# Kernel tuning notes

Hardware: AMD Instinct MI355X
Metric: run time of the kernel (lower is better)

## Reference

```python
import jax, jax.numpy as jnp
import numpy as np

N_QUBITS = 4
N_LAYERS = 2
ENT = [(i, (i + 1) % N_QUBITS) for i in range(N_QUBITS)]  # fixed entangling ring


def _ry(t):
    c, s = jnp.cos(t / 2), jnp.sin(t / 2)
    return jnp.stack([jnp.stack([c, -s]), jnp.stack([s, c])]).astype(jnp.complex64)


def _rx(t):
    c, s = jnp.cos(t / 2), jnp.sin(t / 2)
    return jnp.stack([jnp.stack([c + 0j, -1j * s]), jnp.stack([-1j * s, c + 0j])]).astype(jnp.complex64)


def _rz(t):
    e = jnp.exp(-0.5j * t.astype(jnp.complex64))
    z = jnp.zeros_like(e)
    return jnp.stack([jnp.stack([e, z]), jnp.stack([z, jnp.conj(e)])])


def _apply_1q(state, U, w):
    # state: (2,)*N_QUBITS; apply 2x2 U on wire w
    s = jnp.moveaxis(state, w, 0)
    s = jnp.tensordot(U, s, ((1,), (0,)))
    return jnp.moveaxis(s, 0, w)


def _cnot(state, c, t):
    s = jnp.moveaxis(state, (c, t), (0, 1))
    s = jnp.concatenate([s[:1], jnp.flip(s[1:], axis=1)], axis=0)
    return jnp.moveaxis(s, (0, 1), (c, t))


def _ansatz(state, vec, params):
    for i in range(N_QUBITS):
        state = _apply_1q(state, _ry(vec[i]), i)
    for l in range(N_LAYERS):
        for i in range(N_QUBITS):
            state = _apply_1q(state, _rx(params[l, i, 0]), i)
            state = _apply_1q(state, _ry(params[l, i, 1]), i)
            state = _apply_1q(state, _rz(params[l, i, 2]), i)
        for a_, b_ in ENT:
            state = _cnot(state, a_, b_)
    return state


def _adjoint_ansatz(state, vec, params):
    # inverse gates in reverse order
    for l in reversed(range(N_LAYERS)):
        for a_, b_ in reversed(ENT):
            state = _cnot(state, a_, b_)  # CNOT is self-inverse
        for i in reversed(range(N_QUBITS)):
            state = _apply_1q(state, _rz(-params[l, i, 2]), i)
            state = _apply_1q(state, _ry(-params[l, i, 1]), i)
            state = _apply_1q(state, _rx(-params[l, i, 0]), i)
    for i in reversed(range(N_QUBITS)):
        state = _apply_1q(state, _ry(-vec[i]), i)
    return state


def setup_inputs() -> dict:
    key = jax.random.key(0)
    k1, k2, k3 = jax.random.split(key, 3)
    a = jax.random.normal(k1, (1024, N_QUBITS), dtype=jnp.float32)
    b = jax.random.normal(k2, (1024, N_QUBITS), dtype=jnp.float32)
    params = jax.random.normal(k3, (N_LAYERS, N_QUBITS, 3), dtype=jnp.float32)
    return {"a": a, "b": b, "params": params}


def reference(a, b, params):
    def pair(x, y):
        psi = jnp.zeros((2,) * N_QUBITS, jnp.complex64).at[(0,) * N_QUBITS].set(1.0)
        psi = _ansatz(psi, x, params)
        psi = _adjoint_ansatz(psi, y, params)
        probs = jnp.abs(psi) ** 2
        # expval of PauliZ on wire 0: +1 for |0>, -1 for |1> on axis 0
        z = jnp.sum(probs[0]) - jnp.sum(probs[1])
        return jnp.abs(z)

    # Gram matrix [len(a), len(b)]
    return jax.vmap(lambda x: jax.vmap(lambda y: pair(x, y))(b))(a)
```

## Files before the change

### kernel.cpp

```cpp
#include <hip/hip_runtime.h>


#define NA 1024
#define NB 1024
#define RT2 1.41421356237f

typedef __attribute__((ext_vector_type(8))) short bf16x8;
typedef __attribute__((ext_vector_type(4))) float f32x4;

__device__ __forceinline__ unsigned short f2bf(float x) {
    union { float f; unsigned u; } v; v.f = x;
    unsigned r = v.u + 0x7fffu + ((v.u >> 16) & 1u);
    return (unsigned short)(r >> 16);
}

__device__ __forceinline__ uint4 pack8(const float* f) {
    uint4 u;
    u.x = (unsigned)f2bf(f[0]) | ((unsigned)f2bf(f[1]) << 16);
    u.y = (unsigned)f2bf(f[2]) | ((unsigned)f2bf(f[3]) << 16);
    u.z = (unsigned)f2bf(f[4]) | ((unsigned)f2bf(f[5]) << 16);
    u.w = (unsigned)f2bf(f[6]) | ((unsigned)f2bf(f[7]) << 16);
    return u;
}

__device__ __forceinline__ void ry_gate(float* sr, float* si, int w, float t) {
    float s, c; __sincosf(0.5f * t, &s, &c);
    int st = 8 >> w;
    #pragma unroll
    for (int b = 0; b < 16; ++b) {
        if (b & st) continue;
        int j = b | st;
        float r0 = sr[b], i0 = si[b], r1 = sr[j], i1 = si[j];
        sr[b] = c * r0 - s * r1;  si[b] = c * i0 - s * i1;
        sr[j] = s * r0 + c * r1;  si[j] = s * i0 + c * i1;
    }
}

__device__ __forceinline__ void rx_gate(float* sr, float* si, int w, float t) {
    float s, c; __sincosf(0.5f * t, &s, &c);
    int st = 8 >> w;
    #pragma unroll
    for (int b = 0; b < 16; ++b) {
        if (b & st) continue;
        int j = b | st;
        float r0 = sr[b], i0 = si[b], r1 = sr[j], i1 = si[j];
        sr[b] = c * r0 + s * i1;  si[b] = c * i0 - s * r1;
        sr[j] = c * r1 + s * i0;  si[j] = c * i1 - s * r0;
    }
}

__device__ __forceinline__ void rz_gate(float* sr, float* si, int w, float t) {
    float s, c; __sincosf(0.5f * t, &s, &c);
    int st = 8 >> w;
    #pragma unroll
    for (int b = 0; b < 16; ++b) {
        if (b & st) continue;
        int j = b | st;
        float r0 = sr[b], i0 = si[b], r1 = sr[j], i1 = si[j];
        sr[b] = c * r0 + s * i0;  si[b] = c * i0 - s * r0;
        sr[j] = c * r1 - s * i1;  si[j] = c * i1 + s * r1;
    }
}

__device__ __forceinline__ void cnot_gate(float* sr, float* si, int cw, int tw) {
    int cs = 8 >> cw, ts = 8 >> tw;
    #pragma unroll
    for (int b = 0; b < 16; ++b) {
        if ((b & cs) && !(b & ts)) {
            int j = b | ts;
            float tr = sr[b]; sr[b] = sr[j]; sr[j] = tr;
            float ti = si[b]; si[b] = si[j]; si[j] = ti;
        }
    }
}

__device__ __forceinline__ void ansatz(float* sr, float* si, const float* vec, const float* P) {
    #pragma unroll
    for (int q = 0; q < 4; ++q) ry_gate(sr, si, q, vec[q]);
    #pragma unroll
    for (int l = 0; l < 2; ++l) {
        #pragma unroll
        for (int q = 0; q < 4; ++q) {
            rx_gate(sr, si, q, P[l * 12 + q * 3 + 0]);
            ry_gate(sr, si, q, P[l * 12 + q * 3 + 1]);
            rz_gate(sr, si, q, P[l * 12 + q * 3 + 2]);
        }
        cnot_gate(sr, si, 0, 1);
        cnot_gate(sr, si, 1, 2);
        cnot_gate(sr, si, 2, 3);
        cnot_gate(sr, si, 3, 0);
    }
}

__global__ __launch_bounds__(512, 2) void qkm_fused(
    const float* __restrict__ a, const float* __restrict__ b,
    const float* __restrict__ params, float* __restrict__ out) {

    __shared__ float Wtr[64 * 136];
    __shared__ float Wti[64 * 136];
    __shared__ float Phr[64 * 17];
    __shared__ float Phi_[64 * 17];
    __shared__ __align__(16) char Qsb[32768];
    __shared__ __align__(16) char Msb[32768];

    const int tid = threadIdx.x;
    const int blk = blockIdx.x;
    const int xcd = blk & 7, slot = blk >> 3;
    const int bi = xcd * 2 + (slot >> 4);
    const int bj = slot & 15;
    const int row0 = bi * 64, col0 = bj * 64;

    float P[24];
    #pragma unroll
    for (int j = 0; j < 24; ++j) P[j] = params[j];

    const int y  = tid >> 3;
    const int k2 = tid & 7;
    const int k0 = k2 * 2;
    const int sy = (y & 15) << 4;

    {
        float sr[16], si[16];
        #pragma unroll
        for (int k = 0; k < 16; ++k) { sr[k] = (k == 8 + k2) ? 1.f : 0.f; si[k] = 0.f; }
        float vec[4];
        #pragma unroll
        for (int q = 0; q < 4; ++q) vec[q] = b[(col0 + y) * 4 + q];
        ansatz(sr, si, vec, P);
        float* wr = Wtr + y * 136 + k2 * 17;
        float* wi = Wti + y * 136 + k2 * 17;
        #pragma unroll
        for (int l = 0; l < 16; ++l) { wr[l] = sr[l]; wi[l] = si[l]; }
    }
    __syncthreads();

    if (tid < 64) {
        float sr[16], si[16];
        #pragma unroll
        for (int k = 0; k < 16; ++k) { sr[k] = (k == 0) ? 1.f : 0.f; si[k] = 0.f; }
        float vec[4];
        #pragma unroll
        for (int q = 0; q < 4; ++q) vec[q] = a[(row0 + tid) * 4 + q];
        ansatz(sr, si, vec, P);
        float* qr = Phr + tid * 17;
        float* qi = Phi_ + tid * 17;
        #pragma unroll
        for (int l = 0; l < 16; ++l) { qr[l] = sr[l]; qi[l] = si[l]; }
    }

    {
        const float* wyr = Wtr + y * 136;
        const float* wyi = Wti + y * 136;
        #pragma unroll
        for (int rr = 0; rr < 2; ++rr) {
            const int k = k0 + rr;
            float re[16], im[16];
            #pragma unroll
            for (int l = 0; l < 16; ++l) { re[l] = 0.f; im[l] = 0.f; }
            #pragma unroll
            for (int p2 = 0; p2 < 8; ++p2) {
                const float* br  = wyr + p2 * 17;
                const float* bi_ = wyi + p2 * 17;
                float ar = br[k], ai = bi_[k];
                #pragma unroll
                for (int l = 0; l < 16; ++l) {
                    float xr = br[l], xi = bi_[l];
                    re[l] += ar * xr + ai * xi;
                    im[l] += xi * ar - xr * ai;
                }
            }
            float row[16];
            #pragma unroll
            for (int l = 0; l < 16; ++l) {
                float off = (l < k) ? im[l] : re[l];
                row[l] = (l == k) ? (1.f - 2.f * re[l]) : (-2.f * RT2 * off);
            }
            *(uint4*)(Msb + y * 512 + ((k * 32)      ^ sy)) = pack8(row);
            *(uint4*)(Msb + y * 512 + ((k * 32 + 16) ^ sy)) = pack8(row + 8);
        }
    }
    __syncthreads();

    {
        const float* pr = Phr + y * 17;
        const float* pi = Phi_ + y * 17;
        #pragma unroll
        for (int rr = 0; rr < 2; ++rr) {
            const int k = k0 + rr;
            float rk = pr[k], ik = pi[k];
            float row[16];
            #pragma unroll
            for (int l = 0; l < 16; ++l) {
                float xr = pr[l], xi = pi[l];
                row[l] = (l < k)  ? RT2 * (xi * rk - xr * ik)
                       : (l == k) ? (rk * rk + ik * ik)
                       :            RT2 * (rk * xr + ik * xi);
            }
            *(uint4*)(Qsb + y * 512 + ((k * 32)      ^ sy)) = pack8(row);
            *(uint4*)(Qsb + y * 512 + ((k * 32 + 16) ^ sy)) = pack8(row + 8);
        }
    }
    __syncthreads();

    const int wave = tid >> 6, lane = tid & 63;
    const int wi = wave >> 2, wj = wave & 3;
    const int m16 = lane & 15, quad = lane >> 4;
    const int rA0 = wi * 32 + m16;
    const int rA1 = rA0 + 16;
    const int rB  = wj * 16 + m16;
    const int sA  = m16 << 4;
    const char* qp0 = Qsb + rA0 * 512;
    const char* qp1 = Qsb + rA1 * 512;
    const char* mp  = Msb + rB  * 512;
    f32x4 a0 = {0.f, 0.f, 0.f, 0.f}, a1 = {0.f, 0.f, 0.f, 0.f};
    #pragma unroll
    for (int kk = 0; kk < 8; ++kk) {
        int cb = (kk * 64 + quad * 16) ^ sA;
        bf16x8 qa = *(const bf16x8*)(qp0 + cb);
        bf16x8 qb = *(const bf16x8*)(qp1 + cb);
        bf16x8 ma = *(const bf16x8*)(mp  + cb);
        a0 = __builtin_amdgcn_mfma_f32_16x16x32_bf16(qa, ma, a0, 0, 0, 0);
        a1 = __builtin_amdgcn_mfma_f32_16x16x32_bf16(qb, ma, a1, 0, 0, 0);
    }
    #pragma unroll
    for (int r = 0; r < 4; ++r) {
        int orow = row0 + wi * 32 + quad * 4 + r;
        int ocol = col0 + wj * 16 + m16;
        out[orow * NB + ocol]        = fabsf(a0[r]);
        out[(orow + 16) * NB + ocol] = fabsf(a1[r]);
    }
}

extern "C" void kernel_launch(void* const* d_in, const int* in_sizes, int n_in,
                              void* d_out, int out_size, void* d_ws, size_t ws_size,
                              hipStream_t stream) {
    const float* a = (const float*)d_in[0];
    const float* b = (const float*)d_in[1];
    const float* params = (const float*)d_in[2];
    float* out = (float*)d_out;

    (void)d_ws; (void)ws_size;
    qkm_fused<<<256, 512, 0, stream>>>(a, b, params, out);
}
```

Baseline: 80.86 us.

## Compute feature rows once globally and share via cooperative grid sync

Each block used to recompute the ansatz states and the Q/M feature rows for its own 64 rows and 64 columns, which meant every column state was recomputed 16 times across the grid. Now each block computes features for only 4 rows and 4 columns and writes them as bf16 to a global workspace. A cooperative grid-wide sync follows, after which each block runs its MFMA tile by loading operands straight from global memory instead of LDS. This removes the redundant ansatz and feature work. In exchange it adds a grid barrier, global round trips and a cooperative launch, and it needs the workspace to be large enough.

Result: slower. 181.2 us (+124.1%).

```diff
diff --git a/kernel.cpp b/kernel.cpp
--- a/kernel.cpp
+++ b/kernel.cpp
@@ -1,8 +1,12 @@
 #include <hip/hip_runtime.h>
+#include <hip/hip_cooperative_groups.h>
+
+namespace cg = cooperative_groups;
 
 
 #define NA 1024
 #define NB 1024
+#define KD 256
 #define RT2 1.41421356237f
 
 typedef __attribute__((ext_vector_type(8))) short bf16x8;
@@ -92,142 +96,123 @@
     }
 }
 
-__global__ __launch_bounds__(512, 2) void qkm_fused(
+__global__ __launch_bounds__(512, 2) void qkm_mono(
     const float* __restrict__ a, const float* __restrict__ b,
-    const float* __restrict__ params, float* __restrict__ out) {
-
-    __shared__ float Wtr[64 * 136];
-    __shared__ float Wti[64 * 136];
-    __shared__ float Phr[64 * 17];
-    __shared__ float Phi_[64 * 17];
-    __shared__ __align__(16) char Qsb[32768];
-    __shared__ __align__(16) char Msb[32768];
+    const float* __restrict__ params,
+    unsigned short* __restrict__ Qg, unsigned short* __restrict__ Mg,
+    float* __restrict__ out) {
+
+    __shared__ float Wtr[4 * 136];
+    __shared__ float Wti[4 * 136];
+    __shared__ float Phr[4 * 17];
+    __shared__ float Phi_[4 * 17];
 
     const int tid = threadIdx.x;
     const int blk = blockIdx.x;
+
+    if (tid < 36) {
+        float P[24];
+        #pragma unroll
+        for (int j = 0; j < 24; ++j) P[j] = params[j];
+        int init; const float* src;
+        if (tid < 32) { init = 8 + (tid & 7); src = b + (size_t)(blk * 4 + (tid >> 3)) * 4; }
+        else          { init = 0;             src = a + (size_t)(blk * 4 + (tid - 32)) * 4; }
+        float sr[16], si[16];
+        #pragma unroll
+        for (int k = 0; k < 16; ++k) { sr[k] = (k == init) ? 1.f : 0.f; si[k] = 0.f; }
+        float vec[4];
+        #pragma unroll
+        for (int q = 0; q < 4; ++q) vec[q] = src[q];
+        ansatz(sr, si, vec, P);
+        if (tid < 32) {
+            float* wr = Wtr + (tid >> 3) * 136 + (tid & 7) * 17;
+            float* wi = Wti + (tid >> 3) * 136 + (tid & 7) * 17;
+            #pragma unroll
+            for (int l = 0; l < 16; ++l) { wr[l] = sr[l]; wi[l] = si[l]; }
+        } else {
+            float* qr = Phr + (tid - 32) * 17;
+            float* qi = Phi_ + (tid - 32) * 17;
+            #pragma unroll
+            for (int l = 0; l < 16; ++l) { qr[l] = sr[l]; qi[l] = si[l]; }
+        }
+    }
+    __syncthreads();
+
+    if (tid < 64) {
+        const int yl = tid >> 4, k = tid & 15;
+        const float* wyr = Wtr + yl * 136;
+        const float* wyi = Wti + yl * 136;
+        float re[16], im[16];
+        #pragma unroll
+        for (int l = 0; l < 16; ++l) { re[l] = 0.f; im[l] = 0.f; }
+        #pragma unroll
+        for (int p2 = 0; p2 < 8; ++p2) {
+            const float* br  = wyr + p2 * 17;
+            const float* bi_ = wyi + p2 * 17;
+            float ar = br[k], ai = bi_[k];
+            #pragma unroll
+            for (int l = 0; l < 16; ++l) {
+                float xr = br[l], xi = bi_[l];
+                re[l] += ar * xr + ai * xi;
+                im[l] += xi * ar - xr * ai;
+            }
+        }
+        float row[16];
+        #pragma unroll
+        for (int l = 0; l < 16; ++l) {
+            float off = (l < k) ? im[l] : re[l];
+            row[l] = (l == k) ? (1.f - 2.f * re[l]) : (-2.f * RT2 * off);
+        }
+        uint4* d = (uint4*)Mg + (size_t)(blk * 4 + yl) * 32 + k * 2;
+        d[0] = pack8(row); d[1] = pack8(row + 8);
+    } else if (tid < 128) {
+        const int t2 = tid - 64, il = t2 >> 4, k = t2 & 15;
+        const float* pr = Phr + il * 17;
+        const float* pi = Phi_ + il * 17;
+        float rk = pr[k], ik = pi[k];
+        float row[16];
+        #pragma unroll
+        for (int l = 0; l < 16; ++l) {
+            float xr = pr[l], xi = pi[l];
+            row[l] = (l < k)  ? RT2 * (xi * rk - xr * ik)
+                   : (l == k) ? (rk * rk + ik * ik)
+                   :            RT2 * (rk * xr + ik * xi);
+        }
+        uint4* d = (uint4*)Qg + (size_t)(blk * 4 + il) * 32 + k * 2;
+        d[0] = pack8(row); d[1] = pack8(row + 8);
+    }
+
+    __threadfence();
+    cg::this_grid().sync();
+    __threadfence();
+
+    const int wave = tid >> 6, lane = tid & 63;
     const int xcd = blk & 7, slot = blk >> 3;
     const int bi = xcd * 2 + (slot >> 4);
     const int bj = slot & 15;
-    const int row0 = bi * 64, col0 = bj * 64;
-
-    float P[24];
-    #pragma unroll
-    for (int j = 0; j < 24; ++j) P[j] = params[j];
-
-    const int y  = tid >> 3;
-    const int k2 = tid & 7;
-    const int k0 = k2 * 2;
-    const int sy = (y & 15) << 4;
-
-    {
-        float sr[16], si[16];
-        #pragma unroll
-        for (int k = 0; k < 16; ++k) { sr[k] = (k == 8 + k2) ? 1.f : 0.f; si[k] = 0.f; }
-        float vec[4];
-        #pragma unroll
-        for (int q = 0; q < 4; ++q) vec[q] = b[(col0 + y) * 4 + q];
-        ansatz(sr, si, vec, P);
-        float* wr = Wtr + y * 136 + k2 * 17;
-        float* wi = Wti + y * 136 + k2 * 17;
-        #pragma unroll
-        for (int l = 0; l < 16; ++l) { wr[l] = sr[l]; wi[l] = si[l]; }
-    }
-    __syncthreads();
-
-    if (tid < 64) {
-        float sr[16], si[16];
-        #pragma unroll
-        for (int k = 0; k < 16; ++k) { sr[k] = (k == 0) ? 1.f : 0.f; si[k] = 0.f; }
-        float vec[4];
-        #pragma unroll
-        for (int q = 0; q < 4; ++q) vec[q] = a[(row0 + tid) * 4 + q];
-        ansatz(sr, si, vec, P);
-        float* qr = Phr + tid * 17;
-        float* qi = Phi_ + tid * 17;
-        #pragma unroll
-        for (int l = 0; l < 16; ++l) { qr[l] = sr[l]; qi[l] = si[l]; }
-    }
-
-    {
-        const float* wyr = Wtr + y * 136;
-        const float* wyi = Wti + y * 136;
-        #pragma unroll
-        for (int rr = 0; rr < 2; ++rr) {
-            const int k = k0 + rr;
-            float re[16], im[16];
-            #pragma unroll
-            for (int l = 0; l < 16; ++l) { re[l] = 0.f; im[l] = 0.f; }
-            #pragma unroll
-            for (int p2 = 0; p2 < 8; ++p2) {
-                const float* br  = wyr + p2 * 17;
-                const float* bi_ = wyi + p2 * 17;
-                float ar = br[k], ai = bi_[k];
-                #pragma unroll
-                for (int l = 0; l < 16; ++l) {
-                    float xr = br[l], xi = bi_[l];
-                    re[l] += ar * xr + ai * xi;
-                    im[l] += xi * ar - xr * ai;
-                }
-            }
-            float row[16];
-            #pragma unroll
-            for (int l = 0; l < 16; ++l) {
-                float off = (l < k) ? im[l] : re[l];
-                row[l] = (l == k) ? (1.f - 2.f * re[l]) : (-2.f * RT2 * off);
-            }
-            *(uint4*)(Msb + y * 512 + ((k * 32)      ^ sy)) = pack8(row);
-            *(uint4*)(Msb + y * 512 + ((k * 32 + 16) ^ sy)) = pack8(row + 8);
-        }
-    }
-    __syncthreads();
-
-    {
-        const float* pr = Phr + y * 17;
-        const float* pi = Phi_ + y * 17;
-        #pragma unroll
-        for (int rr = 0; rr < 2; ++rr) {
-            const int k = k0 + rr;
-            float rk = pr[k], ik = pi[k];
-            float row[16];
-            #pragma unroll
-            for (int l = 0; l < 16; ++l) {
-                float xr = pr[l], xi = pi[l];
-                row[l] = (l < k)  ? RT2 * (xi * rk - xr * ik)
-                       : (l == k) ? (rk * rk + ik * ik)
-                       :            RT2 * (rk * xr + ik * xi);
-            }
-            *(uint4*)(Qsb + y * 512 + ((k * 32)      ^ sy)) = pack8(row);
-            *(uint4*)(Qsb + y * 512 + ((k * 32 + 16) ^ sy)) = pack8(row + 8);
-        }
-    }
-    __syncthreads();
-
-    const int wave = tid >> 6, lane = tid & 63;
     const int wi = wave >> 2, wj = wave & 3;
+    const int row0 = bi * 64 + wi * 32;
+    const int col0 = bj * 64 + wj * 16;
     const int m16 = lane & 15, quad = lane >> 4;
-    const int rA0 = wi * 32 + m16;
-    const int rA1 = rA0 + 16;
-    const int rB  = wj * 16 + m16;
-    const int sA  = m16 << 4;
-    const char* qp0 = Qsb + rA0 * 512;
-    const char* qp1 = Qsb + rA1 * 512;
-    const char* mp  = Msb + rB  * 512;
+
+    const unsigned short* q0 = Qg + (size_t)(row0 + m16) * KD + quad * 8;
+    const unsigned short* q1 = q0 + 16 * KD;
+    const unsigned short* m0 = Mg + (size_t)(col0 + m16) * KD + quad * 8;
+
     f32x4 a0 = {0.f, 0.f, 0.f, 0.f}, a1 = {0.f, 0.f, 0.f, 0.f};
     #pragma unroll
     for (int kk = 0; kk < 8; ++kk) {
-        int cb = (kk * 64 + quad * 16) ^ sA;
-        bf16x8 qa = *(const bf16x8*)(qp0 + cb);
-        bf16x8 qb = *(const bf16x8*)(qp1 + cb);
-        bf16x8 ma = *(const bf16x8*)(mp  + cb);
+        bf16x8 qa = *(const bf16x8*)(q0 + kk * 32);
+        bf16x8 qb = *(const bf16x8*)(q1 + kk * 32);
+        bf16x8 ma = *(const bf16x8*)(m0 + kk * 32);
         a0 = __builtin_amdgcn_mfma_f32_16x16x32_bf16(qa, ma, a0, 0, 0, 0);
         a1 = __builtin_amdgcn_mfma_f32_16x16x32_bf16(qb, ma, a1, 0, 0, 0);
     }
     #pragma unroll
     for (int r = 0; r < 4; ++r) {
-        int orow = row0 + wi * 32 + quad * 4 + r;
-        int ocol = col0 + wj * 16 + m16;
-        out[orow * NB + ocol]        = fabsf(a0[r]);
-        out[(orow + 16) * NB + ocol] = fabsf(a1[r]);
+        int orow = row0 + quad * 4 + r;
+        out[orow * NB + col0 + m16]        = fabsf(a0[r]);
+        out[(orow + 16) * NB + col0 + m16] = fabsf(a1[r]);
     }
 }
 
@@ -239,6 +224,11 @@
     const float* params = (const float*)d_in[2];
     float* out = (float*)d_out;
 
-    (void)d_ws; (void)ws_size;
-    qkm_fused<<<256, 512, 0, stream>>>(a, b, params, out);
-}
+    unsigned short* Q = (unsigned short*)d_ws;
+    unsigned short* M = Q + (size_t)NA * KD;
+
+    void* args[] = { (void*)&a, (void*)&b, (void*)&params,
+                     (void*)&Q, (void*)&M, (void*)&out };
+    hipLaunchCooperativeKernel((const void*)qkm_mono, dim3(256), dim3(512),
+                               args, 0, stream);
+}
```
